# Kernel optimization log

Hardware: AMD Instinct MI355X
Metric: run time of the kernel (lower is better)

## Reference

```python
import jax, jax.numpy as jnp
import numpy as np

IN_DIM = 16384; DM = 512; DEPTH = 4
DI = 1024   # d_inner = expand * d_model
DS = 16     # d_state
DC = 4      # d_conv
DR = 32     # dt_rank = ceil(d_model/16)
B = 4; L = 256


def setup_inputs() -> dict:
    key = jax.random.key(0)
    ks = jax.random.split(key, 12)
    g = lambda k, s, sc=0.02: jax.random.normal(k, s, jnp.float32) * sc
    return {
        "x": jax.random.normal(ks[0], (B, L, IN_DIM), jnp.float32),
        # top-level projections / norm
        "in_w": g(ks[1], (DM, IN_DIM)), "in_b": jnp.zeros((DM,), jnp.float32),
        "ln_g": jnp.ones((DM,), jnp.float32), "ln_b": jnp.zeros((DM,), jnp.float32),
        "out_w": g(ks[2], (IN_DIM, DM)), "out_b": jnp.zeros((IN_DIM,), jnp.float32),
        # stacked per-layer Mamba params (leading dim = DEPTH)
        "m_in_w": g(ks[3], (DEPTH, 2 * DI, DM)),
        "conv_w": g(ks[4], (DEPTH, DI, DC), 0.2),
        "conv_b": jnp.zeros((DEPTH, DI), jnp.float32),
        "xproj_w": g(ks[5], (DEPTH, DR + 2 * DS, DI)),
        "dt_w": g(ks[6], (DEPTH, DI, DR), 0.1),
        "dt_b": jax.random.uniform(ks[7], (DEPTH, DI), jnp.float32, -4.0, -2.0),
        "A_log": jnp.log(jnp.broadcast_to(jnp.arange(1, DS + 1, dtype=jnp.float32), (DEPTH, DI, DS))),
        "D_p": jnp.ones((DEPTH, DI), jnp.float32),
        "m_out_w": g(ks[8], (DEPTH, DM, DI)),
    }


def _mamba(h, iw, cw, cb, xw, dw, db, Alog, Dp, ow):
    """One Mamba block (no residual, matching bare mamba_ssm.Mamba)."""
    Bn, Ln, _ = h.shape
    xz = h @ iw.T                                  # [B,L,2*DI]
    xc, z = jnp.split(xz, 2, axis=-1)
    # causal depthwise conv1d, kernel DC, truncated to L
    xp = jnp.pad(xc, ((0, 0), (DC - 1, 0), (0, 0)))
    conv = cb
    for k in range(DC):
        conv = conv + xp[:, k:k + Ln, :] * cw[:, k]
    xc = jax.nn.silu(conv)                         # [B,L,DI]
    xdbl = xc @ xw.T                               # [B,L,DR+2*DS]
    dt, Bm, Cm = xdbl[..., :DR], xdbl[..., DR:DR + DS], xdbl[..., DR + DS:]
    dt = jax.nn.softplus(dt @ dw.T + db)           # [B,L,DI]
    A = -jnp.exp(Alog)                             # [DI,DS]
    dA = jnp.exp(dt[..., None] * A)                # [B,L,DI,DS]
    dBx = dt[..., None] * Bm[:, :, None, :] * xc[..., None]  # [B,L,DI,DS]

    def step(hst, inp):
        a, b, c = inp
        hst = a * hst + b
        return hst, jnp.einsum('bdn,bn->bd', hst, c)

    h0 = jnp.zeros((Bn, DI, DS), xc.dtype)
    _, ys = jax.lax.scan(step, h0, (dA.transpose(1, 0, 2, 3), dBx.transpose(1, 0, 2, 3), Cm.transpose(1, 0, 2)))
    y = ys.transpose(1, 0, 2) + xc * Dp            # [B,L,DI]
    y = y * jax.nn.silu(z)
    return y @ ow.T                                # [B,L,DM]


def reference(x, in_w, in_b, ln_g, ln_b, out_w, out_b, m_in_w, conv_w, conv_b, xproj_w, dt_w, dt_b, A_log, D_p, m_out_w):
    h = x @ in_w.T + in_b                          # [B,L,DM]
    for i in range(DEPTH):
        h = _mamba(h, m_in_w[i], conv_w[i], conv_b[i], xproj_w[i], dt_w[i], dt_b[i], A_log[i], D_p[i], m_out_w[i])
    hl = h[:, -1]                                  # [B,DM]
    mu = hl.mean(-1, keepdims=True)
    var = ((hl - mu) ** 2).mean(-1, keepdims=True)
    hn = (hl - mu) / jnp.sqrt(var + 1e-5) * ln_g + ln_b
    return hn @ out_w.T + out_b                    # [B,IN_DIM]
```

## Files before the change

### kernel.cpp

```cpp
#include <hip/hip_runtime.h>
#include <stdint.h>

#define DEV static __device__ __forceinline__

typedef __attribute__((ext_vector_type(8))) __bf16 bf16x8;
typedef __attribute__((ext_vector_type(4))) float f32x4;

DEV float bfs2f(unsigned short u) {
    union { unsigned int i; float f; } c; c.i = ((unsigned int)u) << 16; return c.f;
}
DEV unsigned short f2bf(float v) {
    union { __bf16 b; unsigned short u; } c; c.b = (__bf16)v; return c.u;
}

template<int TH, int BM, int BN, int BK, int AMODE, int BMODE, int EPI, int CSPLIT, int SWZ>
__global__ __launch_bounds__(TH) void gemm_k(
    const void* __restrict__ A0, const void* __restrict__ A1,
    const void* __restrict__ B0, const void* __restrict__ B1,
    const float* __restrict__ bias,
    float* __restrict__ C0, float* __restrict__ C1,
    int lda, int ldb, int ldc, int Klen, int pstride)
{
    constexpr int NWN = TH / 128;
    constexpr int FM = BM / 2 / 16;
    constexpr int FN = BN / NWN / 16;
    constexpr int KB = BK / 32;
    constexpr int GAF = (AMODE == 0) ? BM * BK / (TH * 4) : 1;
    constexpr int GAP = (AMODE == 1) ? BM * BK / (TH * 8) : 1;
    constexpr int GBF = (BMODE == 0) ? BN * BK / (TH * 4) : 1;
    constexpr int GBP = (BMODE == 1) ? BN * BK / (TH * 8) : 1;

    __shared__ __align__(16) char smem[2 * (BM + BN) * BK * 2];
    char* sAh = smem;
    char* sAl = smem + BM * BK * 2;
    char* sBh = smem + 2 * BM * BK * 2;
    char* sBl = smem + 2 * BM * BK * 2 + BN * BK * 2;

    int bx = blockIdx.x, by = blockIdx.y, bz = blockIdx.z;
    if (SWZ) {
        int lin = blockIdx.x + gridDim.x * (blockIdx.y + gridDim.y * blockIdx.z);
        bz = lin & 7;
        int rest = lin >> 3;
        bx = rest % gridDim.x;
        by = rest / gridDim.x;
    }

    const int tid = threadIdx.x, lane = tid & 63;
    const int wid = tid >> 6;
    const int wm = wid & 1, wn = wid >> 1;
    const int q = lane >> 4, t16 = lane & 15;
    const int tileM = bx * BM, tileN = by * BN;
    const int kBase = bz * Klen, kEnd = kBase + Klen;
    float* C = C0 + (size_t)bz * pstride;

    f32x4 acc[FM][FN];
#pragma unroll
    for (int a = 0; a < FM; ++a)
#pragma unroll
        for (int b = 0; b < FN; ++b) acc[a][b] = f32x4{0.f, 0.f, 0.f, 0.f};

    float4 aF[GAF], bF[GBF];
    int4 aH[GAP], aL[GAP], bH[GBP], bL[GBP];

    auto loadA = [&](int k0) {
        if (AMODE == 0) {
            const float* A32 = (const float*)A0;
#pragma unroll
            for (int u = 0; u < GAF; ++u) {
                int idx = u * TH + tid;
                int r = idx / (BK / 4), c4 = idx % (BK / 4);
                aF[u] = *(const float4*)(A32 + (size_t)(tileM + r) * lda + k0 + c4 * 4);
            }
        } else {
            const unsigned short* Ah = (const unsigned short*)A0;
            const unsigned short* Al = (const unsigned short*)A1;
#pragma unroll
            for (int u = 0; u < GAP; ++u) {
                int idx = u * TH + tid;
                int r = idx / (BK / 8), c8 = idx % (BK / 8);
                size_t src = (size_t)(tileM + r) * lda + k0 + c8 * 8;
                aH[u] = *(const int4*)(Ah + src);
                aL[u] = *(const int4*)(Al + src);
            }
        }
    };
    auto loadB = [&](int k0) {
        if (BMODE == 0) {
            const float* B32 = (const float*)B0;
#pragma unroll
            for (int u = 0; u < GBF; ++u) {
                int idx = u * TH + tid;
                int r = idx / (BK / 4), c4 = idx % (BK / 4);
                bF[u] = *(const float4*)(B32 + (size_t)(tileN + r) * ldb + k0 + c4 * 4);
            }
        } else {
            const unsigned short* Bh = (const unsigned short*)B0;
            const unsigned short* Bl = (const unsigned short*)B1;
#pragma unroll
            for (int u = 0; u < GBP; ++u) {
                int idx = u * TH + tid;
                int r = idx / (BK / 8), c8 = idx % (BK / 8);
                size_t src = (size_t)(tileN + r) * ldb + k0 + c8 * 8;
                bH[u] = *(const int4*)(Bh + src);
                bL[u] = *(const int4*)(Bl + src);
            }
        }
    };
    auto storeA = [&]() {
        if (AMODE == 0) {
#pragma unroll
            for (int u = 0; u < GAF; ++u) {
                int idx = u * TH + tid;
                int r = idx / (BK / 4), c4 = idx % (BK / 4);
                float vv[4] = {aF[u].x, aF[u].y, aF[u].z, aF[u].w};
                ushort4 hv, lv;
                unsigned short* hp = (unsigned short*)&hv;
                unsigned short* lp = (unsigned short*)&lv;
#pragma unroll
                for (int e = 0; e < 4; ++e) {
                    unsigned short hb = f2bf(vv[e]);
                    hp[e] = hb; lp[e] = f2bf(vv[e] - bfs2f(hb));
                }
                int off = (c4 / 8) * BM * 64 + r * 64 + (c4 & 7) * 8;
                *(ushort4*)(sAh + off) = hv;
                *(ushort4*)(sAl + off) = lv;
            }
        } else {
#pragma unroll
            for (int u = 0; u < GAP; ++u) {
                int idx = u * TH + tid;
                int r = idx / (BK / 8), c8 = idx % (BK / 8);
                int off = (c8 / 4) * BM * 64 + r * 64 + (c8 & 3) * 16;
                *(int4*)(sAh + off) = aH[u];
                *(int4*)(sAl + off) = aL[u];
            }
        }
    };
    auto storeB = [&]() {
        if (BMODE == 0) {
#pragma unroll
            for (int u = 0; u < GBF; ++u) {
                int idx = u * TH + tid;
                int r = idx / (BK / 4), c4 = idx % (BK / 4);
                float vv[4] = {bF[u].x, bF[u].y, bF[u].z, bF[u].w};
                ushort4 hv, lv;
                unsigned short* hp = (unsigned short*)&hv;
                unsigned short* lp = (unsigned short*)&lv;
#pragma unroll
                for (int e = 0; e < 4; ++e) {
                    unsigned short hb = f2bf(vv[e]);
                    hp[e] = hb; lp[e] = f2bf(vv[e] - bfs2f(hb));
                }
                int off = (c4 / 8) * BN * 64 + r * 64 + (c4 & 7) * 8;
                *(ushort4*)(sBh + off) = hv;
                *(ushort4*)(sBl + off) = lv;
            }
        } else {
#pragma unroll
            for (int u = 0; u < GBP; ++u) {
                int idx = u * TH + tid;
                int r = idx / (BK / 8), c8 = idx % (BK / 8);
                int off = (c8 / 4) * BN * 64 + r * 64 + (c8 & 3) * 16;
                *(int4*)(sBh + off) = bH[u];
                *(int4*)(sBl + off) = bL[u];
            }
        }
    };

    loadA(kBase); loadB(kBase);
    for (int k0 = kBase; k0 < kEnd; k0 += BK) {
        storeA(); storeB();
        __syncthreads();
        if (k0 + BK < kEnd) { loadA(k0 + BK); loadB(k0 + BK); }
#pragma unroll
        for (int kb = 0; kb < KB; ++kb) {
            bf16x8 ah[FM], al[FM], bh[FN], bl[FN];
#pragma unroll
            for (int fm = 0; fm < FM; ++fm) {
                int off = kb * BM * 64 + (wm * (BM / 2) + fm * 16 + t16) * 64 + q * 16;
                ah[fm] = *(const bf16x8*)(sAh + off);
                al[fm] = *(const bf16x8*)(sAl + off);
            }
#pragma unroll
            for (int fn = 0; fn < FN; ++fn) {
                int off = kb * BN * 64 + (wn * (BN / NWN) + fn * 16 + t16) * 64 + q * 16;
                bh[fn] = *(const bf16x8*)(sBh + off);
                bl[fn] = *(const bf16x8*)(sBl + off);
            }
#pragma unroll
            for (int fm = 0; fm < FM; ++fm)
#pragma unroll
                for (int fn = 0; fn < FN; ++fn) {
                    acc[fm][fn] = __builtin_amdgcn_mfma_f32_16x16x32_bf16(ah[fm], bh[fn], acc[fm][fn], 0, 0, 0);
                    acc[fm][fn] = __builtin_amdgcn_mfma_f32_16x16x32_bf16(al[fm], bh[fn], acc[fm][fn], 0, 0, 0);
                    acc[fm][fn] = __builtin_amdgcn_mfma_f32_16x16x32_bf16(ah[fm], bl[fn], acc[fm][fn], 0, 0, 0);
                }
        }
        __syncthreads();
    }

#pragma unroll
    for (int fm = 0; fm < FM; ++fm) {
        int row0 = tileM + wm * (BM / 2) + fm * 16 + q * 4;
#pragma unroll
        for (int fn = 0; fn < FN; ++fn) {
            int col = tileN + wn * (BN / NWN) + fn * 16 + t16;
            float* Cd = C; int cc2 = col;
            if (CSPLIT && col >= ldc) { Cd = C1; cc2 = col - ldc; }
            float bv = (EPI == 2) ? bias[col] : 0.f;
#pragma unroll
            for (int r = 0; r < 4; ++r) {
                float v = acc[fm][fn][r];
                if (EPI == 2) { v = fminf(v + bv, 60.f); v = log1pf(__expf(v)); }
                Cd[(size_t)(row0 + r) * ldc + cc2] = v;
            }
        }
    }
}

__global__ __launch_bounds__(256) void reduce_k(
    const float* __restrict__ part, int Z, int pstride, int n,
    const float* __restrict__ bias, int colmask,
    unsigned short* __restrict__ hi, unsigned short* __restrict__ lo,
    float* __restrict__ hlast, int colbits)
{
    int i = blockIdx.x * 256 + threadIdx.x;
    if (i >= n) return;
    float s = 0.f;
    for (int z = 0; z < Z; ++z) s += part[(size_t)z * pstride + i];
    if (bias) s += bias[i & colmask];
    unsigned short hb = f2bf(s);
    hi[i] = hb; lo[i] = f2bf(s - bfs2f(hb));
    if (hlast) {
        int row = i >> colbits;
        if ((row & 255) == 255)
            hlast[((row >> 8) << colbits) + (i & colmask)] = s;
    }
}

__global__ __launch_bounds__(256) void conv_silu_k(
    const float* __restrict__ xb, const float* __restrict__ cw,
    const float* __restrict__ cb, unsigned short* __restrict__ xch,
    unsigned short* __restrict__ xcl)
{
    int i  = blockIdx.x * 256 + threadIdx.x;
    int d  = i & 1023;
    int bl = i >> 10;
    int l  = bl & 255;
    float a = cb[d];
#pragma unroll
    for (int k = 0; k < 4; ++k) {
        int ls = l + k - 3;
        if (ls >= 0) a += xb[(size_t)(bl + k - 3) * 1024 + d] * cw[d * 4 + k];
    }
    float v = a / (1.f + __expf(-a));
    unsigned short hb = f2bf(v);
    xch[i] = hb; xcl[i] = f2bf(v - bfs2f(hb));
}

__global__ __launch_bounds__(256) void scan_k(
    const float* __restrict__ zb,
    const unsigned short* __restrict__ xch, const unsigned short* __restrict__ xcl,
    const unsigned short* __restrict__ xdh, const unsigned short* __restrict__ xdl,
    const float* __restrict__ dt, const float* __restrict__ Alog,
    const float* __restrict__ Dp,
    unsigned short* __restrict__ ygh, unsigned short* __restrict__ ygl)
{
    __shared__ float sdt[2048], sxc[2048], szz[2048], sbc[2048];
    int b   = blockIdx.x >> 5;
    int d0  = (blockIdx.x & 31) << 5;
    int ch  = threadIdx.x >> 3;
    int d   = d0 + ch;
    int sub = threadIdx.x & 7;
    int j0  = sub * 2;
    float An[2], hst[2] = {0.f, 0.f};
    An[0] = -__expf(Alog[d * 16 + j0]);
    An[1] = -__expf(Alog[d * 16 + j0 + 1]);
    float Dd  = Dp[d];
    int   bl0 = b * 256;

    for (int c = 0; c < 4; ++c) {
        __syncthreads();
#pragma unroll
        for (int it = 0; it < 8; ++it) {
            int j2 = it * 256 + threadIdx.x;
            int ll = j2 >> 5, dd = j2 & 31;
            size_t row = (size_t)(bl0 + c * 64 + ll);
            size_t gi  = row * 1024 + d0 + dd;
            sdt[j2] = dt[gi];
            sxc[j2] = bfs2f(xch[gi]) + bfs2f(xcl[gi]);
            szz[j2] = zb[gi];
            size_t bi = row * 64 + 32 + dd;
            sbc[j2] = bfs2f(xdh[bi]) + bfs2f(xdl[bi]);
        }
        __syncthreads();
#pragma unroll 4
        for (int li = 0; li < 64; ++li) {
            float dtv = sdt[li * 32 + ch];
            float xcv = sxc[li * 32 + ch];
            float c1  = dtv * xcv;
            float dA0 = __expf(dtv * An[0]);
            float dA1 = __expf(dtv * An[1]);
            float B0  = sbc[li * 32 + j0],      B1 = sbc[li * 32 + j0 + 1];
            float C0  = sbc[li * 32 + 16 + j0], C1 = sbc[li * 32 + 16 + j0 + 1];
            hst[0] = dA0 * hst[0] + c1 * B0;
            hst[1] = dA1 * hst[1] + c1 * B1;
            float y = hst[0] * C0 + hst[1] * C1;
            y += __shfl_xor(y, 1);
            y += __shfl_xor(y, 2);
            y += __shfl_xor(y, 4);
            if (sub == 0) {
                float zv = szz[li * 32 + ch];
                float sg = zv / (1.f + __expf(-zv));
                float v  = (y + xcv * Dd) * sg;
                unsigned short hb = f2bf(v);
                size_t o = (size_t)(bl0 + c * 64 + li) * 1024 + d;
                ygh[o] = hb; ygl[o] = f2bf(v - bfs2f(hb));
            }
        }
    }
}

__global__ __launch_bounds__(512) void ln_k(
    const float* __restrict__ hlast, const float* __restrict__ g,
    const float* __restrict__ bb, float* __restrict__ hn)
{
    __shared__ float red[16];
    int b = blockIdx.x, k = threadIdx.x;
    float x = hlast[b * 512 + k];
    float s = x, s2 = x * x;
#pragma unroll
    for (int m = 32; m; m >>= 1) { s += __shfl_xor(s, m, 64); s2 += __shfl_xor(s2, m, 64); }
    if ((k & 63) == 0) { red[k >> 6] = s; red[8 + (k >> 6)] = s2; }
    __syncthreads();
    float ts = 0.f, ts2 = 0.f;
#pragma unroll
    for (int j = 0; j < 8; ++j) { ts += red[j]; ts2 += red[8 + j]; }
    float mu   = ts * (1.f / 512.f);
    float var  = ts2 * (1.f / 512.f) - mu * mu;
    float rstd = rsqrtf(var + 1e-5f);
    hn[b * 512 + k] = (x - mu) * rstd * g[k] + bb[k];
}

__global__ __launch_bounds__(256) void final_k(
    const float* __restrict__ hn, const float* __restrict__ W,
    const float* __restrict__ ob, float* __restrict__ out)
{
    int wid = threadIdx.x >> 6, lane = threadIdx.x & 63;
    float a[4][8];
#pragma unroll
    for (int b2 = 0; b2 < 4; ++b2) {
        float4 v0 = *(const float4*)&hn[b2 * 512 + lane * 8];
        float4 v1 = *(const float4*)&hn[b2 * 512 + lane * 8 + 4];
        a[b2][0] = v0.x; a[b2][1] = v0.y; a[b2][2] = v0.z; a[b2][3] = v0.w;
        a[b2][4] = v1.x; a[b2][5] = v1.y; a[b2][6] = v1.z; a[b2][7] = v1.w;
    }
#pragma unroll 1
    for (int it = 0; it < 8; ++it) {
        int n = blockIdx.x * 4 + wid + it * 2048;
        const float* W32 = W + (size_t)n * 512 + lane * 8;
        float4 v0 = *(const float4*)W32;
        float4 v1 = *(const float4*)(W32 + 4);
        float wf[8] = {v0.x, v0.y, v0.z, v0.w, v1.x, v1.y, v1.z, v1.w};
        float s0 = 0.f, s1 = 0.f, s2 = 0.f, s3 = 0.f;
#pragma unroll
        for (int j = 0; j < 8; ++j) {
            s0 += a[0][j] * wf[j]; s1 += a[1][j] * wf[j];
            s2 += a[2][j] * wf[j]; s3 += a[3][j] * wf[j];
        }
#pragma unroll
        for (int m = 32; m; m >>= 1) {
            s0 += __shfl_xor(s0, m, 64); s1 += __shfl_xor(s1, m, 64);
            s2 += __shfl_xor(s2, m, 64); s3 += __shfl_xor(s3, m, 64);
        }
        if (lane == 0) {
            float bv = ob[n];
            out[0 * 16384 + n] = s0 + bv;
            out[1 * 16384 + n] = s1 + bv;
            out[2 * 16384 + n] = s2 + bv;
            out[3 * 16384 + n] = s3 + bv;
        }
    }
}

extern "C" void kernel_launch(void* const* d_in, const int* in_sizes, int n_in,
                              void* d_out, int out_size, void* d_ws, size_t ws_size,
                              hipStream_t stream)
{
    const float* x      = (const float*)d_in[0];
    const float* in_w   = (const float*)d_in[1];
    const float* in_b   = (const float*)d_in[2];
    const float* ln_g   = (const float*)d_in[3];
    const float* ln_b   = (const float*)d_in[4];
    const float* out_w  = (const float*)d_in[5];
    const float* out_b  = (const float*)d_in[6];
    const float* m_in_w = (const float*)d_in[7];
    const float* conv_w = (const float*)d_in[8];
    const float* conv_b = (const float*)d_in[9];
    const float* xproj_w= (const float*)d_in[10];
    const float* dt_w   = (const float*)d_in[11];
    const float* dt_b   = (const float*)d_in[12];
    const float* A_log  = (const float*)d_in[13];
    const float* D_p    = (const float*)d_in[14];
    const float* m_out_w= (const float*)d_in[15];

    char* W = (char*)d_ws;
    unsigned short* hplh = (unsigned short*)(W + 0);
    unsigned short* hpll = (unsigned short*)(W + 1048576);
    float* hlast = (float*)(W + 2097152);
    float* hn    = (float*)(W + 2162688);
    float* xbuf  = (float*)(W + 2228224);
    float* zbuf  = (float*)(W + 6422528);
    unsigned short* xch = (unsigned short*)(W + 10616832);
    unsigned short* xcl = (unsigned short*)(W + 12713984);
    float* dtb   = (float*)(W + 14811136);
    unsigned short* xdbh  = (unsigned short*)(W + 19005440);
    unsigned short* xdbl_ = (unsigned short*)(W + 19136512);
    float* part1 = (float*)(W + 2228224);
    float* partx = (float*)(W + 14811136);
    float* parto = (float*)(W + 6422528);
    unsigned short* ygh = (unsigned short*)(W + 2228224);
    unsigned short* ygl = (unsigned short*)(W + 4325376);

    gemm_k<512,128,128,64,0,0,0,0,1><<<dim3(8,4,8),512,0,stream>>>(
        x, nullptr, in_w, nullptr, nullptr, part1, nullptr,
        16384, 16384, 512, 2048, 524288);
    reduce_k<<<2048,256,0,stream>>>(part1, 8, 524288, 524288, in_b, 511,
                                    hplh, hpll, hlast, 9);

    for (int i = 0; i < 4; ++i) {
        const float* iw = m_in_w  + (size_t)i * 1048576;
        const float* cw = conv_w  + (size_t)i * 4096;
        const float* cb = conv_b  + (size_t)i * 1024;
        const float* xw = xproj_w + (size_t)i * 65536;
        const float* dw = dt_w    + (size_t)i * 32768;
        const float* db = dt_b    + (size_t)i * 1024;
        const float* Al = A_log   + (size_t)i * 16384;
        const float* Dp = D_p     + (size_t)i * 1024;
        const float* ow = m_out_w + (size_t)i * 524288;

        gemm_k<512,64,128,64,1,0,0,1,0><<<dim3(16,16,1),512,0,stream>>>(
            hplh, hpll, iw, nullptr, nullptr, xbuf, zbuf, 512, 512, 1024, 512, 0);
        conv_silu_k<<<4096,256,0,stream>>>(xbuf, cw, cb, xch, xcl);
        gemm_k<256,64,64,64,1,0,0,0,0><<<dim3(16,1,16),256,0,stream>>>(
            xch, xcl, xw, nullptr, nullptr, partx, nullptr, 1024, 1024, 64, 64, 65536);
        reduce_k<<<256,256,0,stream>>>(partx, 16, 65536, 65536, nullptr, 63,
                                       xdbh, xdbl_, nullptr, 6);
        gemm_k<256,64,64,32,1,0,2,0,0><<<dim3(16,16,1),256,0,stream>>>(
            xdbh, xdbl_, dw, nullptr, db, dtb, nullptr, 64, 32, 1024, 32, 0);
        scan_k<<<128,256,0,stream>>>(zbuf, xch, xcl, xdbh, xdbl_, dtb, Al, Dp,
                                     ygh, ygl);
        gemm_k<512,64,128,64,1,0,0,0,0><<<dim3(16,4,8),512,0,stream>>>(
            ygh, ygl, ow, nullptr, nullptr, parto, nullptr, 1024, 1024, 512, 128, 524288);
        reduce_k<<<2048,256,0,stream>>>(parto, 8, 524288, 524288, nullptr, 511,
                                        hplh, hpll, hlast, 9);
    }

    ln_k<<<4,512,0,stream>>>(hlast, ln_g, ln_b, hn);
    final_k<<<512,256,0,stream>>>(hn, out_w, out_b, (float*)d_out);
}
```

Measured before the change: 738.3 us.

## Double-buffer LDS in input-projection GEMM and add XCD-aware block swizzles

Adds a DBUF template option that keeps two LDS buffers, so the next K tile is converted and stored while the current one feeds the MFMAs. This removes one __syncthreads per iteration and overlaps global loads with compute. It is enabled only for the large first GEMM (x @ in_w), which doubles that kernel's LDS use to 128 KB and may lower occupancy. It also adds a new swizzle mode that groups N tiles per XCD for the per-layer in-projection GEMM, and turns on the existing split-K swizzle for the out-projection GEMM, both aiming at better L2 locality.

```diff
diff --git a/kernel.cpp b/kernel.cpp
--- a/kernel.cpp
+++ b/kernel.cpp
@@ -13,7 +13,8 @@
     union { __bf16 b; unsigned short u; } c; c.b = (__bf16)v; return c.u;
 }
 
-template<int TH, int BM, int BN, int BK, int AMODE, int BMODE, int EPI, int CSPLIT, int SWZ>
+template<int TH, int BM, int BN, int BK, int AMODE, int BMODE, int EPI,
+         int CSPLIT, int SWZ, int DBUF>
 __global__ __launch_bounds__(TH) void gemm_k(
     const void* __restrict__ A0, const void* __restrict__ A1,
     const void* __restrict__ B0, const void* __restrict__ B1,
@@ -29,20 +30,23 @@
     constexpr int GAP = (AMODE == 1) ? BM * BK / (TH * 8) : 1;
     constexpr int GBF = (BMODE == 0) ? BN * BK / (TH * 4) : 1;
     constexpr int GBP = (BMODE == 1) ? BN * BK / (TH * 8) : 1;
-
-    __shared__ __align__(16) char smem[2 * (BM + BN) * BK * 2];
-    char* sAh = smem;
-    char* sAl = smem + BM * BK * 2;
-    char* sBh = smem + 2 * BM * BK * 2;
-    char* sBl = smem + 2 * BM * BK * 2 + BN * BK * 2;
+    constexpr int BUFB = 2 * (BM + BN) * BK * 2;
+
+    __shared__ __align__(16) char smem[(DBUF ? 2 : 1) * BUFB];
 
     int bx = blockIdx.x, by = blockIdx.y, bz = blockIdx.z;
-    if (SWZ) {
+    if (SWZ == 1) {
         int lin = blockIdx.x + gridDim.x * (blockIdx.y + gridDim.y * blockIdx.z);
         bz = lin & 7;
         int rest = lin >> 3;
         bx = rest % gridDim.x;
         by = rest / gridDim.x;
+    } else if (SWZ == 2) {
+        int lin = blockIdx.x + gridDim.x * blockIdx.y;
+        int xcd = lin & 7, t = lin >> 3;
+        int gpx = gridDim.y / 8;
+        by = xcd * gpx + t % gpx;
+        bx = t / gpx;
     }
 
     const int tid = threadIdx.x, lane = tid & 63;
@@ -106,7 +110,7 @@
             }
         }
     };
-    auto storeA = [&]() {
+    auto storeA = [&](char* sAh, char* sAl) {
         if (AMODE == 0) {
 #pragma unroll
             for (int u = 0; u < GAF; ++u) {
@@ -136,7 +140,7 @@
             }
         }
     };
-    auto storeB = [&]() {
+    auto storeB = [&](char* sBh, char* sBl) {
         if (BMODE == 0) {
 #pragma unroll
             for (int u = 0; u < GBF; ++u) {
@@ -166,12 +170,8 @@
             }
         }
     };
-
-    loadA(kBase); loadB(kBase);
-    for (int k0 = kBase; k0 < kEnd; k0 += BK) {
-        storeA(); storeB();
-        __syncthreads();
-        if (k0 + BK < kEnd) { loadA(k0 + BK); loadB(k0 + BK); }
+    auto compute = [&](const char* sAh, const char* sAl,
+                       const char* sBh, const char* sBl) {
 #pragma unroll
         for (int kb = 0; kb < KB; ++kb) {
             bf16x8 ah[FM], al[FM], bh[FN], bl[FN];
@@ -196,7 +196,38 @@
                     acc[fm][fn] = __builtin_amdgcn_mfma_f32_16x16x32_bf16(ah[fm], bl[fn], acc[fm][fn], 0, 0, 0);
                 }
         }
+    };
+
+    loadA(kBase); loadB(kBase);
+    if (DBUF) {
+        storeA(smem, smem + BM * BK * 2);
+        storeB(smem + 2 * BM * BK * 2, smem + 2 * BM * BK * 2 + BN * BK * 2);
         __syncthreads();
+        int p = 0;
+        for (int k0 = kBase; k0 < kEnd; k0 += BK) {
+            bool more = (k0 + BK < kEnd);
+            if (more) { loadA(k0 + BK); loadB(k0 + BK); }
+            char* cb = smem + p * BUFB;
+            compute(cb, cb + BM * BK * 2,
+                    cb + 2 * BM * BK * 2, cb + 2 * BM * BK * 2 + BN * BK * 2);
+            if (more) {
+                char* nb = smem + (p ^ 1) * BUFB;
+                storeA(nb, nb + BM * BK * 2);
+                storeB(nb + 2 * BM * BK * 2, nb + 2 * BM * BK * 2 + BN * BK * 2);
+            }
+            __syncthreads();
+            p ^= 1;
+        }
+    } else {
+        for (int k0 = kBase; k0 < kEnd; k0 += BK) {
+            storeA(smem, smem + BM * BK * 2);
+            storeB(smem + 2 * BM * BK * 2, smem + 2 * BM * BK * 2 + BN * BK * 2);
+            __syncthreads();
+            if (k0 + BK < kEnd) { loadA(k0 + BK); loadB(k0 + BK); }
+            compute(smem, smem + BM * BK * 2,
+                    smem + 2 * BM * BK * 2, smem + 2 * BM * BK * 2 + BN * BK * 2);
+            __syncthreads();
+        }
     }
 
 #pragma unroll
@@ -422,7 +453,7 @@
     unsigned short* ygh = (unsigned short*)(W + 2228224);
     unsigned short* ygl = (unsigned short*)(W + 4325376);
 
-    gemm_k<512,128,128,64,0,0,0,0,1><<<dim3(8,4,8),512,0,stream>>>(
+    gemm_k<512,128,128,64,0,0,0,0,1,1><<<dim3(8,4,8),512,0,stream>>>(
         x, nullptr, in_w, nullptr, nullptr, part1, nullptr,
         16384, 16384, 512, 2048, 524288);
     reduce_k<<<2048,256,0,stream>>>(part1, 8, 524288, 524288, in_b, 511,
@@ -439,18 +470,18 @@
         const float* Dp = D_p     + (size_t)i * 1024;
         const float* ow = m_out_w + (size_t)i * 524288;
 
-        gemm_k<512,64,128,64,1,0,0,1,0><<<dim3(16,16,1),512,0,stream>>>(
+        gemm_k<512,64,128,64,1,0,0,1,2,0><<<dim3(16,16,1),512,0,stream>>>(
             hplh, hpll, iw, nullptr, nullptr, xbuf, zbuf, 512, 512, 1024, 512, 0);
         conv_silu_k<<<4096,256,0,stream>>>(xbuf, cw, cb, xch, xcl);
-        gemm_k<256,64,64,64,1,0,0,0,0><<<dim3(16,1,16),256,0,stream>>>(
+        gemm_k<256,64,64,64,1,0,0,0,0,0><<<dim3(16,1,16),256,0,stream>>>(
             xch, xcl, xw, nullptr, nullptr, partx, nullptr, 1024, 1024, 64, 64, 65536);
         reduce_k<<<256,256,0,stream>>>(partx, 16, 65536, 65536, nullptr, 63,
                                        xdbh, xdbl_, nullptr, 6);
-        gemm_k<256,64,64,32,1,0,2,0,0><<<dim3(16,16,1),256,0,stream>>>(
+        gemm_k<256,64,64,32,1,0,2,0,0,0><<<dim3(16,16,1),256,0,stream>>>(
             xdbh, xdbl_, dw, nullptr, db, dtb, nullptr, 64, 32, 1024, 32, 0);
         scan_k<<<128,256,0,stream>>>(zbuf, xch, xcl, xdbh, xdbl_, dtb, Al, Dp,
                                      ygh, ygl);
-        gemm_k<512,64,128,64,1,0,0,0,0><<<dim3(16,4,8),512,0,stream>>>(
+        gemm_k<512,64,128,64,1,0,0,0,1,0><<<dim3(16,4,8),512,0,stream>>>(
             ygh, ygl, ow, nullptr, nullptr, parto, nullptr, 1024, 1024, 512, 128, 524288);
         reduce_k<<<2048,256,0,stream>>>(parto, 8, 524288, 524288, nullptr, 511,
                                         hplh, hpll, hlast, 9);
```

Measured after the change: 765.0 us. 3.6% more time.
